# Kernel tuning notes

Hardware: AMD Instinct MI355X
Metric: run time of the kernel (lower is better)

Reference implementation:

```python
import jax, jax.numpy as jnp
import numpy as np

B, S, H, NH, HD = 4, 2048, 2048, 16, 128
SCALE = HD ** -0.5


def rotate_half(x):
    x1, x2 = jnp.split(x, 2, axis=-1)
    return jnp.concatenate([-x2, x1], axis=-1)


def setup_inputs() -> dict:
    key = jax.random.key(0)
    ks = jax.random.split(key, 8)
    x = jax.random.normal(ks[0], (B, S, H), dtype=jnp.float32)
    # RoPE tables for positions 0..S-1, standard theta=10000 construction
    inv_freq = 1.0 / (10000.0 ** (jnp.arange(0, HD, 2, dtype=jnp.float32) / HD))
    t = jnp.arange(S, dtype=jnp.float32)
    freqs = jnp.einsum('s,d->sd', t, inv_freq)          # [S, HD/2]
    emb = jnp.concatenate([freqs, freqs], axis=-1)      # [S, HD]
    cos, sin = jnp.cos(emb), jnp.sin(emb)
    # causal mask: True = masked (future positions)
    mask = jnp.triu(jnp.ones((S, S), dtype=bool), k=1)
    std = H ** -0.5
    Wq = jax.random.normal(ks[1], (H, H), dtype=jnp.float32) * std
    Wk = jax.random.normal(ks[2], (H, H), dtype=jnp.float32) * std
    Wv = jax.random.normal(ks[3], (H, H), dtype=jnp.float32) * std
    Wo = jax.random.normal(ks[4], (H, H), dtype=jnp.float32) * std
    return {"x": x, "cos": cos, "sin": sin, "mask": mask,
            "Wq": Wq, "Wk": Wk, "Wv": Wv, "Wo": Wo}


def reference(x, cos, sin, mask, Wq, Wk, Wv, Wo):
    # projections: nn.Linear(bias=False) => x @ W.T
    def proj(W):
        y = jnp.einsum('bsh,ih->bsi', x, W)             # [B,S,inner]
        return y.reshape(B, S, NH, HD).transpose(0, 2, 1, 3)  # [B,NH,S,HD]
    q, k, v = proj(Wq), proj(Wk), proj(Wv)
    # RoPE (rotate-half), cos/sin broadcast over batch & heads
    c = cos[None, None, :, :]
    s = sin[None, None, :, :]
    q = q * c + rotate_half(q) * s
    k = k * c + rotate_half(k) * s
    # attention
    attn = jnp.einsum('bhqd,bhkd->bhqk', q, k) * SCALE
    attn = jnp.where(mask[None, None, :, :], -jnp.inf, attn)
    attn = jax.nn.softmax(attn, axis=-1)
    out = jnp.einsum('bhqk,bhkd->bhqd', attn, v)
    out = out.transpose(0, 2, 1, 3).reshape(B, S, NH * HD)
    y = jnp.einsum('bsi,hi->bsh', out, Wo)
    return y, k, v
```

## Files before the change

kernel.cpp:

```cpp
#include <hip/hip_runtime.h>
#include <hip/hip_bf16.h>
#include <math.h>

typedef __bf16 bf16_t;
typedef __bf16 bf16x8 __attribute__((ext_vector_type(8)));
typedef __bf16 bf16x4v __attribute__((ext_vector_type(4)));
typedef float  f32x4  __attribute__((ext_vector_type(4)));
typedef float  f32x16 __attribute__((ext_vector_type(16)));
typedef unsigned int u32x4 __attribute__((ext_vector_type(4)));

constexpr int CB = 4, CS = 2048, CH = 2048, CNH = 16, CHD = 128;
constexpr int CM = CB * CS;
constexpr float CSCALE = 0.08838834764831845f;
constexpr float CL2E   = 1.4426950408889634f;
constexpr float CSC2   = CSCALE * CL2E;

__device__ __forceinline__ float fexp2(float x) {
  float r;
  asm("v_exp_f32 %0, %1" : "=v"(r) : "v"(x));
  return r;
}

__device__ __forceinline__ void g2l16(const void* g, void* l) {
  __builtin_amdgcn_global_load_lds(
      (const __attribute__((address_space(1))) void*)g,
      (__attribute__((address_space(3))) void*)l, 16, 0, 0);
}

__global__ __launch_bounds__(256) void cvt_all(const float* __restrict__ x,
                                               const float* __restrict__ Wq,
                                               const float* __restrict__ Wk,
                                               const float* __restrict__ Wv,
                                               const float* __restrict__ Wo,
                                               bf16_t* __restrict__ xb,
                                               bf16_t* __restrict__ wqb,
                                               bf16_t* __restrict__ wkb,
                                               bf16_t* __restrict__ wvb,
                                               bf16_t* __restrict__ wob) {
  constexpr int NX = CM * CH / 4;
  constexpr int NW = CH * CH / 4;
  const int i = blockIdx.x * 256 + threadIdx.x;
  const float* src;
  bf16_t* dst;
  int off;
  if (i < NX) {
    src = x; dst = xb; off = i;
  } else {
    const int j = i - NX;
    const int sel = j / NW;
    off = j - sel * NW;
    src = (sel == 0) ? Wq : (sel == 1) ? Wk : (sel == 2) ? Wv : Wo;
    dst = (sel == 0) ? wqb : (sel == 1) ? wkb : (sel == 2) ? wvb : wob;
  }
  float4 v = reinterpret_cast<const float4*>(src)[off];
  bf16x4v o = {(bf16_t)v.x, (bf16_t)v.y, (bf16_t)v.z, (bf16_t)v.w};
  reinterpret_cast<bf16x4v*>(dst)[off] = o;
}

__device__ __forceinline__ void gemm256sq_core(const bf16_t* __restrict__ A,
                                               const bf16_t* __restrict__ Bm,
                                               bf16_t (*As2)[4][64 * 64],
                                               bf16_t (*Bs2)[4][64 * 64],
                                               int row0, int col0,
                                               f32x4 (&acc)[8][4]) {
  const int tid = threadIdx.x, lane = tid & 63, w = tid >> 6;
  const int wm = w >> 2, wn = w & 3;
  constexpr int NKT = CH / 64;
  const int id = w * 64 + lane;
  const int rl = id >> 3, ck = id & 7;

  auto stA = [&](int buf, int kt, int q) {
    const int row = q * 64 + rl;
    g2l16(A + (size_t)(row0 + row) * CH + kt * 64 + ((ck ^ (row & 7)) << 3),
          &As2[buf][q][id * 8]);
  };
  auto stB = [&](int buf, int kt, int q) {
    const int row = q * 64 + rl;
    g2l16(Bm + (size_t)(col0 + row) * CH + kt * 64 + ((ck ^ (row & 7)) << 3),
          &Bs2[buf][q][id * 8]);
  };
  auto rdA = [&](int buf, int r, int c) -> bf16x8 {
    return *(const bf16x8*)(&As2[buf][r >> 6][(r & 63) * 64 + ((c ^ (r & 7)) << 3)]);
  };
  auto rdB = [&](int buf, int r, int c) -> bf16x8 {
    return *(const bf16x8*)(&Bs2[buf][r >> 6][(r & 63) * 64 + ((c ^ (r & 7)) << 3)]);
  };

#pragma unroll
  for (int q = 0; q < 4; ++q) stB(0, 0, q);
#pragma unroll
  for (int q = 0; q < 4; ++q) stA(0, 0, q);
  asm volatile("s_waitcnt vmcnt(0)" ::: "memory");
  __builtin_amdgcn_s_barrier();
  __builtin_amdgcn_sched_barrier(0);

  const int ar0 = wm * 128 + (lane & 15);
  const int br0 = wn * 64 + (lane & 15);
  const int chi = lane >> 4;

  for (int t = 0; t < NKT; ++t) {
    const int buf = t & 1, nbuf = buf ^ 1;
    const bool pf = (t + 1 < NKT);
    bf16x8 bb[4][2], aa[2][2];

#pragma unroll
    for (int p = 0; p < 4; ++p) {
      if (p == 0) {
#pragma unroll
        for (int nf = 0; nf < 4; ++nf)
#pragma unroll
          for (int kk = 0; kk < 2; ++kk)
            bb[nf][kk] = rdB(buf, br0 + nf * 16, kk * 4 + chi);
      }
#pragma unroll
      for (int i = 0; i < 2; ++i)
#pragma unroll
        for (int kk = 0; kk < 2; ++kk)
          aa[i][kk] = rdA(buf, ar0 + (2 * p + i) * 16, kk * 4 + chi);

      if (pf) {
        if (p == 0) { stB(nbuf, t + 1, 0); stB(nbuf, t + 1, 1); }
        if (p == 1) { stB(nbuf, t + 1, 2); stB(nbuf, t + 1, 3); }
        if (p == 2) { stA(nbuf, t + 1, 0); stA(nbuf, t + 1, 2); }
        if (p == 3) { stA(nbuf, t + 1, 1); stA(nbuf, t + 1, 3); }
      }

      __builtin_amdgcn_s_barrier();
      asm volatile("s_waitcnt lgkmcnt(0)" ::: "memory");
      __builtin_amdgcn_sched_barrier(0);
      __builtin_amdgcn_s_setprio(1);
#pragma unroll
      for (int i = 0; i < 2; ++i)
#pragma unroll
        for (int nf = 0; nf < 4; ++nf)
#pragma unroll
          for (int kk = 0; kk < 2; ++kk)
            acc[2 * p + i][nf] = __builtin_amdgcn_mfma_f32_16x16x32_bf16(
                aa[i][kk], bb[nf][kk], acc[2 * p + i][nf], 0, 0, 0);
      __builtin_amdgcn_s_setprio(0);

      if (p == 1) {
        if (pf) { asm volatile("s_waitcnt vmcnt(4)" ::: "memory"); }
        else    { asm volatile("s_waitcnt vmcnt(0)" ::: "memory"); }
      }
      if (p == 3 && pf) { asm volatile("s_waitcnt vmcnt(2)" ::: "memory"); }
      __builtin_amdgcn_s_barrier();
      __builtin_amdgcn_sched_barrier(0);
    }
  }
}

__global__ __launch_bounds__(512, 1) void qkv_gemm(const bf16_t* __restrict__ xb,
                                                   const bf16_t* __restrict__ wqb,
                                                   const bf16_t* __restrict__ wkb,
                                                   const bf16_t* __restrict__ wvb,
                                                   bf16_t* __restrict__ qraw,
                                                   bf16_t* __restrict__ knat,
                                                   bf16_t* __restrict__ vt2,
                                                   float* __restrict__ vout) {
  __shared__ __align__(16) bf16_t LSD[2][2][4][64 * 64];
  const int z = blockIdx.z;
  const bf16_t* Bm = (z == 0) ? wqb : ((z == 1) ? wkb : wvb);
  const int row0 = blockIdx.x * 256, col0 = blockIdx.y * 256;
  f32x4 acc[8][4] = {};
  gemm256sq_core(xb, Bm, LSD[0], LSD[1], row0, col0, acc);

  const int tid = threadIdx.x, lane = tid & 63, w = tid >> 6;
  const int wm = w >> 2, wn = w & 3;

  if (z == 2) {
#pragma unroll
    for (int i = 0; i < 8; ++i) {
#pragma unroll
      for (int j = 0; j < 4; ++j) {
        const int gr0 = row0 + wm * 128 + i * 16 + (lane >> 4) * 4;
        const int gc = col0 + wn * 64 + j * 16 + (lane & 15);
        const int b = gr0 >> 11, s0 = gr0 & (CS - 1);
        const int nh = gc >> 7, hd = gc & (CHD - 1);
        const int bh = b * CNH + nh;
#pragma unroll
        for (int r = 0; r < 4; ++r) {
          const size_t idx = ((size_t)bh * CS + s0 + r) * CHD + hd;
          vout[idx] = acc[i][j][r];
        }
        bf16x4v pv = {(bf16_t)acc[i][j][0], (bf16_t)acc[i][j][1],
                      (bf16_t)acc[i][j][2], (bf16_t)acc[i][j][3]};
        *(bf16x4v*)(vt2 + (((size_t)bh * (CS / 16) + (s0 >> 4)) * CHD + hd) * 16 +
                    (s0 & 15)) = pv;
      }
    }
    return;
  }

  bf16_t* L = &LSD[0][0][0][0];
#pragma unroll
  for (int i = 0; i < 8; ++i)
#pragma unroll
    for (int j = 0; j < 4; ++j) {
      const int col = wn * 64 + j * 16 + (lane & 15);
#pragma unroll
      for (int r = 0; r < 4; ++r) {
        const int row = wm * 128 + i * 16 + (lane >> 4) * 4 + r;
        L[row * 256 + (((col >> 3) ^ (row & 31)) << 3) + (col & 7)] =
            (bf16_t)acc[i][j][r];
      }
    }
  __syncthreads();

  if (z == 0) {
#pragma unroll
    for (int k = 0; k < 16; ++k) {
      const int u = k * 512 + tid;
      const int row = u >> 5, ch = u & 31;
      bf16x8 v = *(const bf16x8*)&L[row * 256 + ((ch ^ (row & 31)) << 3)];
      const int gr = row0 + row, gc = col0 + ch * 8;
      const int b = gr >> 11, s = gr & (CS - 1), nh = gc >> 7, hd = gc & (CHD - 1);
      *(bf16x8*)&qraw[((size_t)(b * CNH + nh) * CS + s) * CHD + hd] = v;
    }
  } else {
#pragma unroll
    for (int k = 0; k < 16; ++k) {
      const int u = k * 512 + tid;
      const int s = u & 255, cc = u >> 8;
      bf16x8 v = *(const bf16x8*)&L[s * 256 + ((cc ^ (s & 31)) << 3)];
      const int gr = row0 + s, gc = col0 + cc * 8;
      const int b = gr >> 11, sg = gr & (CS - 1), nh = gc >> 7, hd = gc & (CHD - 1);
      const int pan = hd >> 4, half = (hd >> 3) & 1;
      *(bf16x8*)&knat[(((size_t)(b * CNH + nh) * 8 + pan) * CS + sg) * 16 +
                      half * 8] = v;
    }
  }
}

__global__ __launch_bounds__(512, 1) void y_gemm(const bf16_t* __restrict__ ob,
                                                 const bf16_t* __restrict__ wob,
                                                 float* __restrict__ yout) {
  __shared__ __align__(16) bf16_t As2[2][4][64 * 64];
  __shared__ __align__(16) bf16_t Bs2[2][4][64 * 64];
  const int row0 = blockIdx.x * 256, col0 = blockIdx.y * 256;
  f32x4 acc[8][4] = {};
  gemm256sq_core(ob, wob, As2, Bs2, row0, col0, acc);
  const int lane = threadIdx.x & 63, w = threadIdx.x >> 6;
  const int wm = w >> 2, wn = w & 3;
#pragma unroll
  for (int i = 0; i < 8; ++i)
#pragma unroll
    for (int j = 0; j < 4; ++j)
#pragma unroll
      for (int r = 0; r < 4; ++r) {
        const int gr = row0 + wm * 128 + i * 16 + (lane >> 4) * 4 + r;
        const int gc = col0 + wn * 64 + j * 16 + (lane & 15);
        yout[(size_t)gr * CH + gc] = acc[i][j][r];
      }
}

__global__ __launch_bounds__(256) void rope_k(bf16_t* __restrict__ knat,
                                              const float* __restrict__ cosd,
                                              const float* __restrict__ sind,
                                              float* __restrict__ kout) {
  const int gid = blockIdx.x * 256 + threadIdx.x;
  const int row = gid >> 3, sub = gid & 7;
  const int pan = sub >> 1, hf = (sub & 1) * 8;
  const int bh = row >> 11, s = row & (CS - 1);
  const int d0 = pan * 16 + hf;
  bf16_t* k1 = knat + (((size_t)bh * 8 + pan) * CS + s) * 16 + hf;
  bf16_t* k2 = knat + (((size_t)bh * 8 + pan + 4) * CS + s) * 16 + hf;
  bf16x8 v1 = *(bf16x8*)k1;
  bf16x8 v2 = *(bf16x8*)k2;
  float c[8], sn[8];
  *(float4*)(c)      = *(const float4*)(cosd + s * CHD + d0);
  *(float4*)(c + 4)  = *(const float4*)(cosd + s * CHD + d0 + 4);
  *(float4*)(sn)     = *(const float4*)(sind + s * CHD + d0);
  *(float4*)(sn + 4) = *(const float4*)(sind + s * CHD + d0 + 4);
  float f1[8], f2[8];
  bf16x8 o1, o2;
#pragma unroll
  for (int i = 0; i < 8; ++i) {
    const float x1 = (float)v1[i], x2 = (float)v2[i];
    f1[i] = x1 * c[i] - x2 * sn[i];
    f2[i] = x2 * c[i] + x1 * sn[i];
    o1[i] = (bf16_t)f1[i];
    o2[i] = (bf16_t)f2[i];
  }
  *(bf16x8*)k1 = o1;
  *(bf16x8*)k2 = o2;
  const size_t kb = (size_t)row * CHD + d0;
  *(float4*)(kout + kb)          = *(float4*)(f1);
  *(float4*)(kout + kb + 4)      = *(float4*)(f1 + 4);
  *(float4*)(kout + kb + 64)     = *(float4*)(f2);
  *(float4*)(kout + kb + 64 + 4) = *(float4*)(f2 + 4);
}

__global__ __launch_bounds__(256) void attn_kernel(const bf16_t* __restrict__ qb,
                                                   const bf16_t* __restrict__ kn,
                                                   const bf16_t* __restrict__ v2,
                                                   const float* __restrict__ cosd,
                                                   const float* __restrict__ sind,
                                                   bf16_t* __restrict__ ob) {
  __shared__ float Os[3][32][129];
  __shared__ float Ms[3][32], Ls[3][32];
  const int tid = threadIdx.x, lane = tid & 63, wh = tid >> 6;
  const int hi = lane >> 5, l31 = lane & 31;

  const int swz = (blockIdx.x & 7) * 512 + (blockIdx.x >> 3);
  const int bh = swz >> 6;
  const int qt = 63 - (swz & 63);

  const int b = bh >> 4, nh = bh & (CNH - 1);
  const bf16_t* kbase = kn + (size_t)bh * 8 * CS * 16;
  const bf16_t* vbase = v2 + (size_t)bh * (CS / 16) * CHD * 16;
  const int qw0 = qt * 32;
  const int qrow = qw0 + l31;

  bf16x8 bq[8];
  {
    const bf16_t* qp = qb + ((size_t)bh * CS + qrow) * CHD + hi * 8;
    bf16x8 raw[8];
#pragma unroll
    for (int ks = 0; ks < 8; ++ks) raw[ks] = *(const bf16x8*)(qp + ks * 16);
#pragma unroll
    for (int p = 0; p < 4; ++p) {
      const int d0 = p * 16 + hi * 8;
      float cc[8], ss[8];
      *(float4*)(cc)     = *(const float4*)(cosd + (size_t)qrow * CHD + d0);
      *(float4*)(cc + 4) = *(const float4*)(cosd + (size_t)qrow * CHD + d0 + 4);
      *(float4*)(ss)     = *(const float4*)(sind + (size_t)qrow * CHD + d0);
      *(float4*)(ss + 4) = *(const float4*)(sind + (size_t)qrow * CHD + d0 + 4);
#pragma unroll
      for (int e = 0; e < 8; ++e) {
        const float x1 = (float)raw[p][e], x2 = (float)raw[p + 4][e];
        bq[p][e]     = (bf16_t)(x1 * cc[e] - x2 * ss[e]);
        bq[p + 4][e] = (bf16_t)(x2 * cc[e] + x1 * ss[e]);
      }
    }
  }

  float m_ = -INFINITY, l_ = 0.f;
  f32x16 o_[4] = {};

  const int nt = (qt >> 1) + 1;
  for (int kt = wh; kt < nt; kt += 4) {
    const int kvb = kt * 64;

    f32x16 st[2] = {};
#pragma unroll
    for (int kb2 = 0; kb2 < 2; ++kb2) {
      const bf16_t* kr = kbase + (size_t)(kvb + kb2 * 32 + l31) * 16 + hi * 8;
#pragma unroll
      for (int ks = 0; ks < 8; ++ks) {
        bf16x8 ak = *(const bf16x8*)(kr + (size_t)ks * CS * 16);
        st[kb2] = __builtin_amdgcn_mfma_f32_32x32x16_bf16(ak, bq[ks], st[kb2], 0, 0, 0);
      }
    }

    const bool anymask = (kvb + 63) > qw0;
#pragma unroll
    for (int blk = 0; blk < 2; ++blk)
#pragma unroll
      for (int r = 0; r < 16; ++r) {
        float xv = st[blk][r] * CSC2;
        if (anymask) {
          const int kv = kvb + blk * 32 + 4 * hi + (r & 3) + 8 * (r >> 2);
          if (kv > qrow) xv = -INFINITY;
        }
        st[blk][r] = xv;
      }

    float tmax = st[0][0];
#pragma unroll
    for (int r = 1; r < 16; ++r) tmax = fmaxf(tmax, st[0][r]);
#pragma unroll
    for (int r = 0; r < 16; ++r) tmax = fmaxf(tmax, st[1][r]);
    tmax = fmaxf(tmax, __shfl_xor(tmax, 32, 64));

    if (__any(tmax - m_ > 8.0f)) {
      const float mn = fmaxf(m_, tmax);
      const float corr = fexp2(m_ - mn);
      m_ = mn;
      l_ *= corr;
#pragma unroll
      for (int hb = 0; hb < 4; ++hb) o_[hb] *= corr;
    }

    float psum = 0.f;
#pragma unroll
    for (int blk = 0; blk < 2; ++blk)
#pragma unroll
      for (int r = 0; r < 16; ++r) {
        const float pv = fexp2(st[blk][r] - m_);
        st[blk][r] = pv;
        psum += pv;
      }
    psum += __shfl_xor(psum, 32, 64);
    l_ += psum;

    bf16x8 pb[4];
#pragma unroll
    for (int ks = 0; ks < 4; ++ks) {
      const int blk = ks >> 1, r0 = (ks & 1) * 8;
      unsigned pw0, pw1, pw2, pw3;
      asm("v_cvt_pk_bf16_f32 %0, %1, %2" : "=v"(pw0) : "v"(st[blk][r0 + 0]), "v"(st[blk][r0 + 1]));
      asm("v_cvt_pk_bf16_f32 %0, %1, %2" : "=v"(pw2) : "v"(st[blk][r0 + 4]), "v"(st[blk][r0 + 5]));
      asm("v_cvt_pk_bf16_f32 %0, %1, %2" : "=v"(pw1) : "v"(st[blk][r0 + 2]), "v"(st[blk][r0 + 3]));
      asm("v_cvt_pk_bf16_f32 %0, %1, %2" : "=v"(pw3) : "v"(st[blk][r0 + 6]), "v"(st[blk][r0 + 7]));
      asm("v_permlane32_swap_b32 %0, %1" : "+v"(pw0), "+v"(pw2));
      asm("v_permlane32_swap_b32 %0, %1" : "+v"(pw1), "+v"(pw3));
      u32x4 pk = {pw0, pw1, pw2, pw3};
      pb[ks] = *reinterpret_cast<bf16x8*>(&pk);
    }

#pragma unroll
    for (int hb = 0; hb < 4; ++hb) {
      const bf16_t* vr = vbase + ((size_t)(kvb >> 4) * CHD + hb * 32 + l31) * 16 + hi * 8;
#pragma unroll
      for (int ks = 0; ks < 4; ++ks) {
        bf16x8 av = *(const bf16x8*)(vr + (size_t)ks * CHD * 16);
        o_[hb] = __builtin_amdgcn_mfma_f32_32x32x16_bf16(av, pb[ks], o_[hb], 0, 0, 0);
      }
    }
  }

  if (wh != 0) {
#pragma unroll
    for (int hb = 0; hb < 4; ++hb)
#pragma unroll
      for (int r = 0; r < 16; ++r) {
        const int hd = 32 * hb + 4 * hi + (r & 3) + 8 * (r >> 2);
        Os[wh - 1][l31][hd] = o_[hb][r];
      }
    if (hi == 0) { Ms[wh - 1][l31] = m_; Ls[wh - 1][l31] = l_; }
  }
  __builtin_amdgcn_s_barrier();
  if (wh != 0) return;

  const float m1 = Ms[0][l31], m2 = Ms[1][l31], m3 = Ms[2][l31];
  const float mn = fmaxf(fmaxf(m_, m1), fmaxf(m2, m3));
  const float c0 = fexp2(m_ - mn), c1 = fexp2(m1 - mn);
  const float c2 = fexp2(m2 - mn), c3 = fexp2(m3 - mn);
  const float linv =
      1.0f / (l_ * c0 + Ls[0][l31] * c1 + Ls[1][l31] * c2 + Ls[2][l31] * c3);
  bf16_t* orow = ob + ((size_t)(b * CS + qrow)) * CH + nh * CHD;
#pragma unroll
  for (int hb = 0; hb < 4; ++hb)
#pragma unroll
    for (int g = 0; g < 4; ++g) {
      const int hd0 = 32 * hb + 4 * hi + 8 * g;
      bf16x4v pv;
#pragma unroll
      for (int e = 0; e < 4; ++e) {
        const float val = o_[hb][4 * g + e] * c0 + Os[0][l31][hd0 + e] * c1 +
                          Os[1][l31][hd0 + e] * c2 + Os[2][l31][hd0 + e] * c3;
        pv[e] = (bf16_t)(val * linv);
      }
      *(bf16x4v*)(orow + hd0) = pv;
    }
}

extern "C" void kernel_launch(void* const* d_in, const int* in_sizes, int n_in,
                              void* d_out, int out_size, void* d_ws, size_t ws_size,
                              hipStream_t stream) {
  const float* x    = (const float*)d_in[0];
  const float* cosd = (const float*)d_in[1];
  const float* sind = (const float*)d_in[2];
  const float* Wq = (const float*)d_in[4];
  const float* Wk = (const float*)d_in[5];
  const float* Wv = (const float*)d_in[6];
  const float* Wo = (const float*)d_in[7];

  float* yout = (float*)d_out;
  float* kout = yout + (size_t)CM * CH;
  float* vout = kout + (size_t)CM * CH;

  char* ws = (char*)d_ws;
  size_t off = 0;
  auto wsalloc = [&](size_t bytes) {
    void* p = ws + off;
    off += (bytes + 255) & ~(size_t)255;
    return p;
  };
  bf16_t* xb   = (bf16_t*)wsalloc((size_t)CM * CH * 2);
  bf16_t* wqb  = (bf16_t*)wsalloc((size_t)CH * CH * 2);
  bf16_t* wkb  = (bf16_t*)wsalloc((size_t)CH * CH * 2);
  bf16_t* wvb  = (bf16_t*)wsalloc((size_t)CH * CH * 2);
  bf16_t* wob  = (bf16_t*)wsalloc((size_t)CH * CH * 2);
  bf16_t* qraw = (bf16_t*)wsalloc((size_t)CM * CH * 2);
  bf16_t* knat = (bf16_t*)wsalloc((size_t)CM * CH * 2);
  bf16_t* vt2  = (bf16_t*)wsalloc((size_t)CM * CH * 2);
  bf16_t* ob   = (bf16_t*)wsalloc((size_t)CM * CH * 2);

  cvt_all<<<(CM * CH / 4 + 4 * CH * CH / 4) / 256, 256, 0, stream>>>(
      x, Wq, Wk, Wv, Wo, xb, wqb, wkb, wvb, wob);

  qkv_gemm<<<dim3(CM / 256, CH / 256, 3), 512, 0, stream>>>(xb, wqb, wkb, wvb,
                                                            qraw, knat, vt2, vout);
  rope_k<<<CB * CNH * CS * 8 / 256, 256, 0, stream>>>(knat, cosd, sind, kout);
  attn_kernel<<<CB * CNH * (CS / 32), 256, 0, stream>>>(qraw, knat, vt2, cosd,
                                                        sind, ob);
  y_gemm<<<dim3(CM / 256, CH / 256), 512, 0, stream>>>(ob, wob, yout);
}
```

Before: 523.4 us.

## Fuse K RoPE into QKV GEMM epilogue and halve attention waves per block

```diff
diff --git a/kernel.cpp b/kernel.cpp
--- a/kernel.cpp
+++ b/kernel.cpp
@@ -154,9 +154,12 @@
                                                    const bf16_t* __restrict__ wqb,
                                                    const bf16_t* __restrict__ wkb,
                                                    const bf16_t* __restrict__ wvb,
+                                                   const float* __restrict__ cosd,
+                                                   const float* __restrict__ sind,
                                                    bf16_t* __restrict__ qraw,
                                                    bf16_t* __restrict__ knat,
                                                    bf16_t* __restrict__ vt2,
+                                                   float* __restrict__ kout,
                                                    float* __restrict__ vout) {
   __shared__ __align__(16) bf16_t LSD[2][2][4][64 * 64];
   const int z = blockIdx.z;
@@ -221,13 +224,45 @@
 #pragma unroll
     for (int k = 0; k < 16; ++k) {
       const int u = k * 512 + tid;
+      const int row = u >> 5, ch = u & 31;
+      bf16x8 v = *(const bf16x8*)&L[row * 256 + ((ch ^ (row & 31)) << 3)];
+      bf16x8 p = *(const bf16x8*)&L[row * 256 + (((ch ^ 8) ^ (row & 31)) << 3)];
+      const int gr = row0 + row, gc = col0 + ch * 8;
+      const int b = gr >> 11, s = gr & (CS - 1), nh = gc >> 7, hd = gc & (CHD - 1);
+      const float sgn = (hd < 64) ? -1.f : 1.f;
+      float c[8], sn[8], o[8];
+      *(float4*)(c)      = *(const float4*)(cosd + (size_t)s * CHD + hd);
+      *(float4*)(c + 4)  = *(const float4*)(cosd + (size_t)s * CHD + hd + 4);
+      *(float4*)(sn)     = *(const float4*)(sind + (size_t)s * CHD + hd);
+      *(float4*)(sn + 4) = *(const float4*)(sind + (size_t)s * CHD + hd + 4);
+#pragma unroll
+      for (int e = 0; e < 8; ++e)
+        o[e] = (float)v[e] * c[e] + sgn * (float)p[e] * sn[e];
+      float* kp = kout + ((size_t)(b * CNH + nh) * CS + s) * CHD + hd;
+      *(float4*)(kp)     = *(float4*)(o);
+      *(float4*)(kp + 4) = *(float4*)(o + 4);
+    }
+#pragma unroll
+    for (int k = 0; k < 16; ++k) {
+      const int u = k * 512 + tid;
       const int s = u & 255, cc = u >> 8;
       bf16x8 v = *(const bf16x8*)&L[s * 256 + ((cc ^ (s & 31)) << 3)];
+      bf16x8 p = *(const bf16x8*)&L[s * 256 + (((cc ^ 8) ^ (s & 31)) << 3)];
       const int gr = row0 + s, gc = col0 + cc * 8;
       const int b = gr >> 11, sg = gr & (CS - 1), nh = gc >> 7, hd = gc & (CHD - 1);
+      const float sgn = (hd < 64) ? -1.f : 1.f;
+      float c[8], sn[8];
+      *(float4*)(c)      = *(const float4*)(cosd + (size_t)sg * CHD + hd);
+      *(float4*)(c + 4)  = *(const float4*)(cosd + (size_t)sg * CHD + hd + 4);
+      *(float4*)(sn)     = *(const float4*)(sind + (size_t)sg * CHD + hd);
+      *(float4*)(sn + 4) = *(const float4*)(sind + (size_t)sg * CHD + hd + 4);
+      bf16x8 o;
+#pragma unroll
+      for (int e = 0; e < 8; ++e)
+        o[e] = (bf16_t)((float)v[e] * c[e] + sgn * (float)p[e] * sn[e]);
       const int pan = hd >> 4, half = (hd >> 3) & 1;
       *(bf16x8*)&knat[(((size_t)(b * CNH + nh) * 8 + pan) * CS + sg) * 16 +
-                      half * 8] = v;
+                      half * 8] = o;
     }
   }
 }
@@ -254,51 +289,14 @@
       }
 }
 
-__global__ __launch_bounds__(256) void rope_k(bf16_t* __restrict__ knat,
-                                              const float* __restrict__ cosd,
-                                              const float* __restrict__ sind,
-                                              float* __restrict__ kout) {
-  const int gid = blockIdx.x * 256 + threadIdx.x;
-  const int row = gid >> 3, sub = gid & 7;
-  const int pan = sub >> 1, hf = (sub & 1) * 8;
-  const int bh = row >> 11, s = row & (CS - 1);
-  const int d0 = pan * 16 + hf;
-  bf16_t* k1 = knat + (((size_t)bh * 8 + pan) * CS + s) * 16 + hf;
-  bf16_t* k2 = knat + (((size_t)bh * 8 + pan + 4) * CS + s) * 16 + hf;
-  bf16x8 v1 = *(bf16x8*)k1;
-  bf16x8 v2 = *(bf16x8*)k2;
-  float c[8], sn[8];
-  *(float4*)(c)      = *(const float4*)(cosd + s * CHD + d0);
-  *(float4*)(c + 4)  = *(const float4*)(cosd + s * CHD + d0 + 4);
-  *(float4*)(sn)     = *(const float4*)(sind + s * CHD + d0);
-  *(float4*)(sn + 4) = *(const float4*)(sind + s * CHD + d0 + 4);
-  float f1[8], f2[8];
-  bf16x8 o1, o2;
-#pragma unroll
-  for (int i = 0; i < 8; ++i) {
-    const float x1 = (float)v1[i], x2 = (float)v2[i];
-    f1[i] = x1 * c[i] - x2 * sn[i];
-    f2[i] = x2 * c[i] + x1 * sn[i];
-    o1[i] = (bf16_t)f1[i];
-    o2[i] = (bf16_t)f2[i];
-  }
-  *(bf16x8*)k1 = o1;
-  *(bf16x8*)k2 = o2;
-  const size_t kb = (size_t)row * CHD + d0;
-  *(float4*)(kout + kb)          = *(float4*)(f1);
-  *(float4*)(kout + kb + 4)      = *(float4*)(f1 + 4);
-  *(float4*)(kout + kb + 64)     = *(float4*)(f2);
-  *(float4*)(kout + kb + 64 + 4) = *(float4*)(f2 + 4);
-}
-
-__global__ __launch_bounds__(256) void attn_kernel(const bf16_t* __restrict__ qb,
+__global__ __launch_bounds__(128) void attn_kernel(const bf16_t* __restrict__ qb,
                                                    const bf16_t* __restrict__ kn,
                                                    const bf16_t* __restrict__ v2,
                                                    const float* __restrict__ cosd,
                                                    const float* __restrict__ sind,
                                                    bf16_t* __restrict__ ob) {
-  __shared__ float Os[3][32][129];
-  __shared__ float Ms[3][32], Ls[3][32];
+  __shared__ float Os[32][129];
+  __shared__ float Ms[32], Ls[32];
   const int tid = threadIdx.x, lane = tid & 63, wh = tid >> 6;
   const int hi = lane >> 5, l31 = lane & 31;
 
@@ -339,18 +337,33 @@
   f32x16 o_[4] = {};
 
   const int nt = (qt >> 1) + 1;
-  for (int kt = wh; kt < nt; kt += 4) {
+  for (int kt = wh; kt < nt; kt += 2) {
     const int kvb = kt * 64;
 
-    f32x16 st[2] = {};
+    bf16x8 ak[2][8];
 #pragma unroll
     for (int kb2 = 0; kb2 < 2; ++kb2) {
       const bf16_t* kr = kbase + (size_t)(kvb + kb2 * 32 + l31) * 16 + hi * 8;
 #pragma unroll
-      for (int ks = 0; ks < 8; ++ks) {
-        bf16x8 ak = *(const bf16x8*)(kr + (size_t)ks * CS * 16);
-        st[kb2] = __builtin_amdgcn_mfma_f32_32x32x16_bf16(ak, bq[ks], st[kb2], 0, 0, 0);
-      }
+      for (int ks = 0; ks < 8; ++ks)
+        ak[kb2][ks] = *(const bf16x8*)(kr + (size_t)ks * CS * 16);
+    }
+
+    f32x16 st[2] = {};
+#pragma unroll
+    for (int kb2 = 0; kb2 < 2; ++kb2)
+#pragma unroll
+      for (int ks = 0; ks < 8; ++ks)
+        st[kb2] = __builtin_amdgcn_mfma_f32_32x32x16_bf16(ak[kb2][ks], bq[ks],
+                                                          st[kb2], 0, 0, 0);
+
+    bf16x8 av[4][4];
+#pragma unroll
+    for (int hb = 0; hb < 4; ++hb) {
+      const bf16_t* vr = vbase + ((size_t)(kvb >> 4) * CHD + hb * 32 + l31) * 16 + hi * 8;
+#pragma unroll
+      for (int ks = 0; ks < 4; ++ks)
+        av[hb][ks] = *(const bf16x8*)(vr + (size_t)ks * CHD * 16);
     }
 
     const bool anymask = (kvb + 63) > qw0;
@@ -410,48 +423,41 @@
     }
 
 #pragma unroll
-    for (int hb = 0; hb < 4; ++hb) {
-      const bf16_t* vr = vbase + ((size_t)(kvb >> 4) * CHD + hb * 32 + l31) * 16 + hi * 8;
-#pragma unroll
-      for (int ks = 0; ks < 4; ++ks) {
-        bf16x8 av = *(const bf16x8*)(vr + (size_t)ks * CHD * 16);
-        o_[hb] = __builtin_amdgcn_mfma_f32_32x32x16_bf16(av, pb[ks], o_[hb], 0, 0, 0);
-      }
-    }
-  }
-
-  if (wh != 0) {
+    for (int hb = 0; hb < 4; ++hb)
+#pragma unroll
+      for (int ks = 0; ks < 4; ++ks)
+        o_[hb] = __builtin_amdgcn_mfma_f32_32x32x16_bf16(av[hb][ks], pb[ks],
+                                                         o_[hb], 0, 0, 0);
+  }
+
+  if (wh == 1) {
 #pragma unroll
     for (int hb = 0; hb < 4; ++hb)
 #pragma unroll
       for (int r = 0; r < 16; ++r) {
         const int hd = 32 * hb + 4 * hi + (r & 3) + 8 * (r >> 2);
-        Os[wh - 1][l31][hd] = o_[hb][r];
-      }
-    if (hi == 0) { Ms[wh - 1][l31] = m_; Ls[wh - 1][l31] = l_; }
+        Os[l31][hd] = o_[hb][r];
+      }
+    if (hi == 0) { Ms[l31] = m_; Ls[l31] = l_; }
   }
   __builtin_amdgcn_s_barrier();
-  if (wh != 0) return;
-
-  const float m1 = Ms[0][l31], m2 = Ms[1][l31], m3 = Ms[2][l31];
-  const float mn = fmaxf(fmaxf(m_, m1), fmaxf(m2, m3));
+  if (wh == 1) return;
+
+  const float m1 = Ms[l31], l1 = Ls[l31];
+  const float mn = fmaxf(m_, m1);
   const float c0 = fexp2(m_ - mn), c1 = fexp2(m1 - mn);
-  const float c2 = fexp2(m2 - mn), c3 = fexp2(m3 - mn);
-  const float linv =
-      1.0f / (l_ * c0 + Ls[0][l31] * c1 + Ls[1][l31] * c2 + Ls[2][l31] * c3);
+  const float linv = 1.0f / (l_ * c0 + l1 * c1);
   bf16_t* orow = ob + ((size_t)(b * CS + qrow)) * CH + nh * CHD;
 #pragma unroll
   for (int hb = 0; hb < 4; ++hb)
 #pragma unroll
     for (int g = 0; g < 4; ++g) {
       const int hd0 = 32 * hb + 4 * hi + 8 * g;
-      bf16x4v pv;
-#pragma unroll
-      for (int e = 0; e < 4; ++e) {
-        const float val = o_[hb][4 * g + e] * c0 + Os[0][l31][hd0 + e] * c1 +
-                          Os[1][l31][hd0 + e] * c2 + Os[2][l31][hd0 + e] * c3;
-        pv[e] = (bf16_t)(val * linv);
-      }
+      bf16x4v pv = {
+          (bf16_t)((o_[hb][4 * g + 0] * c0 + Os[l31][hd0 + 0] * c1) * linv),
+          (bf16_t)((o_[hb][4 * g + 1] * c0 + Os[l31][hd0 + 1] * c1) * linv),
+          (bf16_t)((o_[hb][4 * g + 2] * c0 + Os[l31][hd0 + 2] * c1) * linv),
+          (bf16_t)((o_[hb][4 * g + 3] * c0 + Os[l31][hd0 + 3] * c1) * linv)};
       *(bf16x4v*)(orow + hd0) = pv;
     }
 }
@@ -491,10 +497,9 @@
   cvt_all<<<(CM * CH / 4 + 4 * CH * CH / 4) / 256, 256, 0, stream>>>(
       x, Wq, Wk, Wv, Wo, xb, wqb, wkb, wvb, wob);
 
-  qkv_gemm<<<dim3(CM / 256, CH / 256, 3), 512, 0, stream>>>(xb, wqb, wkb, wvb,
-                                                            qraw, knat, vt2, vout);
-  rope_k<<<CB * CNH * CS * 8 / 256, 256, 0, stream>>>(knat, cosd, sind, kout);
-  attn_kernel<<<CB * CNH * (CS / 32), 256, 0, stream>>>(qraw, knat, vt2, cosd,
+  qkv_gemm<<<dim3(CM / 256, CH / 256, 3), 512, 0, stream>>>(
+      xb, wqb, wkb, wvb, cosd, sind, qraw, knat, vt2, kout, vout);
+  attn_kernel<<<CB * CNH * (CS / 32), 128, 0, stream>>>(qraw, knat, vt2, cosd,
                                                         sind, ob);
   y_gemm<<<dim3(CM / 256, CH / 256), 512, 0, stream>>>(ob, wob, yout);
 }
```

New measurement: 506.2 us. 1.03x faster.
